# Kernel tuning notes

Hardware: AMD Instinct MI355X
Metric: run time of the kernel (lower is better)

Reference implementation:

```python
import jax, jax.numpy as jnp
import numpy as np

N = 4096          # nodes
E = 131072        # edges (avg degree 32)
D_IN = 128        # node_dim
H = 256           # hidden_dim
HEADS = 8
DH = H // HEADS


def setup_inputs() -> dict:
    key = jax.random.key(0)
    ks = jax.random.split(key, 24)
    w = lambda k, shape: (jax.random.normal(k, shape, dtype=jnp.float32) * 0.05)
    inp = {
        "x": jax.random.normal(ks[0], (N, D_IN), dtype=jnp.float32),
        "edge_index": jax.random.randint(ks[1], (2, E), 0, N, dtype=jnp.int32),
        # GCN conv weights (PyG GCNConv: out = aggr(norm * x @ W) + b)
        "W1": w(ks[2], (D_IN, H)), "b1": jnp.zeros((H,), jnp.float32),
        "W2": w(ks[3], (H, H)),    "b2": jnp.zeros((H,), jnp.float32),
        "W3": w(ks[4], (H, H)),    "b3": jnp.zeros((H,), jnp.float32),
        # nn.MultiheadAttention params (torch layout: y = x @ W.T + b)
        "in_w": w(ks[5], (3 * H, H)), "in_b": jnp.zeros((3 * H,), jnp.float32),
        "out_w": w(ks[6], (H, H)),    "out_b": jnp.zeros((H,), jnp.float32),
        # failure_predictor MLP: H -> H/2 -> 3
        "fp1_w": w(ks[7], (H // 2, H)), "fp1_b": jnp.zeros((H // 2,), jnp.float32),
        "fp2_w": w(ks[8], (3, H // 2)), "fp2_b": jnp.zeros((3,), jnp.float32),
        # pattern_detector MLP: H -> H/2 -> 10
        "pd1_w": w(ks[9], (H // 2, H)),  "pd1_b": jnp.zeros((H // 2,), jnp.float32),
        "pd2_w": w(ks[10], (10, H // 2)), "pd2_b": jnp.zeros((10,), jnp.float32),
    }
    return inp


def gcn_conv(x, src, dst, W, b):
    """PyG GCNConv with self-loops and symmetric normalization."""
    h = x @ W                                   # [N, H]
    deg = jnp.zeros((N,), x.dtype).at[dst].add(1.0) + 1.0   # +1 for self-loop
    dinv = jax.lax.rsqrt(deg)
    norm = dinv[src] * dinv[dst]                # [E]
    agg = jnp.zeros_like(h).at[dst].add(h[src] * norm[:, None])
    agg = agg + h * (1.0 / deg)[:, None]        # self-loop term: deg^-1/2 * deg^-1/2
    return agg + b


def mha(h, in_w, in_b, out_w, out_b):
    qkv = h @ in_w.T + in_b                     # [N, 3H]
    q, k, v = jnp.split(qkv, 3, axis=-1)
    q = q.reshape(N, HEADS, DH).transpose(1, 0, 2)   # [h, N, dh]
    k = k.reshape(N, HEADS, DH).transpose(1, 0, 2)
    v = v.reshape(N, HEADS, DH).transpose(1, 0, 2)
    scores = jnp.einsum("hnd,hmd->hnm", q, k) / np.sqrt(DH)
    attn = jax.nn.softmax(scores, axis=-1)
    o = jnp.einsum("hnm,hmd->hnd", attn, v)          # [h, N, dh]
    o = o.transpose(1, 0, 2).reshape(N, H)
    return o @ out_w.T + out_b


def reference(x, edge_index, W1, b1, W2, b2, W3, b3, in_w, in_b, out_w, out_b,
              fp1_w, fp1_b, fp2_w, fp2_b, pd1_w, pd1_b, pd2_w, pd2_b):
    src, dst = edge_index[0], edge_index[1]
    h = jax.nn.relu(gcn_conv(x, src, dst, W1, b1))   # dropout is identity in eval
    h = jax.nn.relu(gcn_conv(h, src, dst, W2, b2))
    h = gcn_conv(h, src, dst, W3, b3)
    h = h + mha(h, in_w, in_b, out_w, out_b)
    risk = jax.nn.softmax(jax.nn.relu(h @ fp1_w.T + fp1_b) @ fp2_w.T + fp2_b, axis=-1)
    patterns = jax.nn.sigmoid(jax.nn.relu(h @ pd1_w.T + pd1_b) @ pd2_w.T + pd2_b)
    return risk, patterns
```

## Files before the change

### kernel.cpp

```cpp
#include <hip/hip_runtime.h>
#include <math.h>

static constexpr int NNODE = 4096;
static constexpr int HDIM  = 256;
static constexpr int DIN   = 128;
static constexpr int HEADS = 8;
static constexpr int SPLIT = 2;

using short8 = __attribute__((ext_vector_type(8))) short;
using f32x4  = __attribute__((ext_vector_type(4))) float;

__device__ inline unsigned short bfr(float x) {
    union { float f; unsigned u; } v; v.f = x;
    unsigned r = v.u + 0x7FFFu + ((v.u >> 16) & 1u);
    return (unsigned short)(r >> 16);
}
__device__ inline unsigned cvt_pk_bf16(float lo, float hi) {
    unsigned r;
    asm("v_cvt_pk_bf16_f32 %0, %1, %2" : "=v"(r) : "v"(lo), "v"(hi));
    return r;
}

__global__ void k_deg(const int* __restrict__ ei, int* __restrict__ degi, int E) {
    int e = blockIdx.x * 256 + threadIdx.x;
    if (e < E) atomicAdd(&degi[ei[E + e]], 1);
}

__global__ __launch_bounds__(256) void k_scan_norm(const int* __restrict__ degi,
        int* __restrict__ off, int* __restrict__ cursor,
        float* __restrict__ dinv, float* __restrict__ invdeg) {
    __shared__ int partial[256];
    __shared__ int basesh[256];
    int t = threadIdx.x;
    int local[16];
    int s = 0;
    #pragma unroll
    for (int i = 0; i < 16; ++i) { local[i] = degi[t * 16 + i]; s += local[i]; }
    partial[t] = s;
    __syncthreads();
    if (t == 0) {
        int run = 0;
        for (int i = 0; i < 256; ++i) { basesh[i] = run; run += partial[i]; }
    }
    __syncthreads();
    int b = basesh[t];
    #pragma unroll
    for (int i = 0; i < 16; ++i) {
        int n = t * 16 + i;
        off[n] = b; cursor[n] = b; b += local[i];
        float d = (float)local[i] + 1.0f;
        dinv[n]   = rsqrtf(d);
        invdeg[n] = 1.0f / d;
    }
}

__global__ void k_fill(const int* __restrict__ ei, int* __restrict__ cursor,
                       int* __restrict__ csr, int E) {
    int e = blockIdx.x * 256 + threadIdx.x;
    if (e < E) {
        int d = ei[E + e];
        int p = atomicAdd(&cursor[d], 1);
        csr[p] = ei[e];
    }
}

__global__ __launch_bounds__(256) void k_prep(
        const float* __restrict__ W1, const float* __restrict__ W2,
        const float* __restrict__ W3, const float* __restrict__ in_w,
        const float* __restrict__ outw, const float* __restrict__ fp1w,
        const float* __restrict__ pd1w, const float* __restrict__ fp1b,
        const float* __restrict__ pd1b,
        unsigned short* __restrict__ W1t, unsigned short* __restrict__ W2t,
        unsigned short* __restrict__ W3t, unsigned short* __restrict__ in_wb,
        unsigned short* __restrict__ outwb, unsigned short* __restrict__ wcatb,
        float* __restrict__ bcat) {
    int idx = blockIdx.x * 256 + threadIdx.x;
    if (idx < 32768) {
        int c = idx >> 7, k = idx & 127;
        W1t[idx] = bfr(W1[(size_t)k * 256 + c]);
    } else if (idx < 98304) {
        int j = idx - 32768; int c = j >> 8, k = j & 255;
        W2t[j] = bfr(W2[(size_t)k * 256 + c]);
    } else if (idx < 163840) {
        int j = idx - 98304; int c = j >> 8, k = j & 255;
        W3t[j] = bfr(W3[(size_t)k * 256 + c]);
    } else if (idx < 360448) {
        int j = idx - 163840;
        in_wb[j] = bfr(in_w[j]);
    } else if (idx < 425984) {
        int j = idx - 360448;
        outwb[j] = bfr(outw[j]);
    } else {
        int j = idx - 425984;
        int row = j >> 8, k = j & 255;
        wcatb[j] = bfr(row < 128 ? fp1w[(size_t)row * 256 + k]
                                 : pd1w[(size_t)(row - 128) * 256 + k]);
        if (j < 256) bcat[j] = (j < 128) ? fp1b[j] : pd1b[j - 128];
    }
}

__global__ __launch_bounds__(256) void k_cvt_x(const float* __restrict__ x,
                                               unsigned short* __restrict__ xb) {
    int i = (blockIdx.x * 256 + threadIdx.x) * 8;
    float4 a = *(const float4*)&x[i];
    float4 b = *(const float4*)&x[i + 4];
    short8 o;
    o[0]=(short)bfr(a.x); o[1]=(short)bfr(a.y); o[2]=(short)bfr(a.z); o[3]=(short)bfr(a.w);
    o[4]=(short)bfr(b.x); o[5]=(short)bfr(b.y); o[6]=(short)bfr(b.z); o[7]=(short)bfr(b.w);
    *(short8*)&xb[i] = o;
}

template<int K, int EPI, bool BIAS, bool ADD>
__global__ __launch_bounds__(256) void k_bgemm(
        const unsigned short* __restrict__ A, const unsigned short* __restrict__ B,
        const float* __restrict__ bias, const float* __restrict__ addsrc,
        void* __restrict__ P0, void* __restrict__ P1, void* __restrict__ P2,
        int Nout) {
    const int lane = threadIdx.x & 63, wave = threadIdx.x >> 6;
    const int ql = lane & 15, g = lane >> 4;
    const int m0w = blockIdx.y * 64 + wave * 16;
    const int n0 = blockIdx.x * 64;
    const unsigned short* ap = A + (size_t)(m0w + ql) * K + g * 8;
    const unsigned short* bp = B + (size_t)(n0 + ql) * K + g * 8;

    f32x4 acc[4] = {{0,0,0,0},{0,0,0,0},{0,0,0,0},{0,0,0,0}};
    #pragma unroll 4
    for (int k0 = 0; k0 < K; k0 += 32) {
        short8 a = *(const short8*)(ap + k0);
        #pragma unroll
        for (int nt = 0; nt < 4; ++nt) {
            short8 b = *(const short8*)(bp + (size_t)nt * 16 * K + k0);
            acc[nt] = __builtin_amdgcn_mfma_f32_16x16x32_bf16(a, b, acc[nt], 0, 0, 0);
        }
    }
    #pragma unroll
    for (int nt = 0; nt < 4; ++nt) {
        const int col = n0 + nt * 16 + ql;
        const float bv = BIAS ? bias[col] : 0.f;
        if (EPI == 2) {
            const int sec = col >> 8, cc = col & 255;
            const int head = cc >> 5, dh = cc & 31;
            unsigned short* dst = (unsigned short*)(sec == 0 ? P0 : (sec == 1 ? P1 : P2));
            const float sc = (sec == 0) ? 0.17677669529663687f : 1.0f;
            #pragma unroll
            for (int i = 0; i < 4; ++i) {
                int row = m0w + g * 4 + i;
                dst[((size_t)head * NNODE + row) * 32 + dh] = bfr((acc[nt][i] + bv) * sc);
            }
        } else if (EPI == 1) {
            unsigned short* Cb = (unsigned short*)P0;
            #pragma unroll
            for (int i = 0; i < 4; ++i) {
                int row = m0w + g * 4 + i;
                float v = acc[nt][i] + bv;
                if (ADD) v += addsrc[(size_t)row * Nout + col];
                Cb[(size_t)row * Nout + col] = bfr(v);
            }
        } else {
            float* Cf = (float*)P0;
            #pragma unroll
            for (int i = 0; i < 4; ++i) {
                int row = m0w + g * 4 + i;
                float v = acc[nt][i] + bv;
                if (ADD) v += addsrc[(size_t)row * Nout + col];
                Cf[(size_t)row * Nout + col] = v;
            }
        }
    }
}

template<int MODE>
__global__ __launch_bounds__(256) void k_gather(const float* __restrict__ hW,
        const int* __restrict__ csr, const int* __restrict__ off,
        const int* __restrict__ degi, const float* __restrict__ dinv,
        const float* __restrict__ invdeg, const float* __restrict__ bias,
        float* __restrict__ aggf, unsigned short* __restrict__ aggb) {
    const int n = blockIdx.x;
    const int c = threadIdx.x;
    const int start = off[n];
    const int cnt = degi[n];
    __shared__ int   sidx[64];
    __shared__ float swht[64];
    float acc = 0.f;
    for (int k0 = 0; k0 < cnt; k0 += 64) {
        __syncthreads();
        if (c < 64 && k0 + c < cnt) {
            int s = csr[start + k0 + c];
            sidx[c] = s;
            swht[c] = dinv[s];
        }
        __syncthreads();
        int lim = min(64, cnt - k0);
        for (int k = 0; k < lim; ++k)
            acc += hW[(size_t)sidx[k] * HDIM + c] * swht[k];
    }
    float val = acc * dinv[n] + hW[(size_t)n * HDIM + c] * invdeg[n] + bias[c];
    if (MODE == 0) {
        aggb[(size_t)n * HDIM + c] = bfr(fmaxf(val, 0.f));
    } else {
        aggf[(size_t)n * HDIM + c] = val;
        aggb[(size_t)n * HDIM + c] = bfr(val);
    }
}

__global__ __launch_bounds__(256) void k_attn_mfma(const unsigned short* __restrict__ qh,
        const unsigned short* __restrict__ kh, const unsigned short* __restrict__ vh,
        float* __restrict__ po, float* __restrict__ pm, float* __restrict__ pl) {
    const int hd = blockIdx.x;
    const int qb = blockIdx.y;
    const int z  = blockIdx.z;
    const int tid = threadIdx.x;
    const int wave = tid >> 6, lane = tid & 63;
    const int ql = lane & 15, g = lane >> 4;

    __shared__ unsigned short Klds[64 * 40];
    __shared__ unsigned short Vt[32 * 72];
    __shared__ unsigned short Plds[4][16 * 72];

    const unsigned short* khh = kh + (size_t)hd * NNODE * 32;
    const unsigned short* vhh = vh + (size_t)hd * NNODE * 32;
    const int row = qb * 64 + wave * 16 + ql;

    short8 qf = *(const short8*)(qh + ((size_t)hd * NNODE + row) * 32 + g * 8);

    f32x4 oa0 = {0,0,0,0}, oa1 = {0,0,0,0};
    float m = -INFINITY, l = 0.f;

    const int skey = tid >> 2, sdh = (tid & 3) * 8;
    const int vkey = tid & 63, vdh = (tid >> 6) * 8;

    const int t0 = z * (NNODE / 64 / SPLIT);
    const int t1 = t0 + (NNODE / 64 / SPLIT);
    for (int kt = t0; kt < t1; ++kt) {
        __syncthreads();
        {
            short8 kv = *(const short8*)(khh + (size_t)(kt * 64 + skey) * 32 + sdh);
            *(short8*)&Klds[skey * 40 + sdh] = kv;
            short8 vv = *(const short8*)(vhh + (size_t)(kt * 64 + vkey) * 32 + vdh);
            #pragma unroll
            for (int i = 0; i < 8; ++i)
                Vt[(vdh + i) * 72 + vkey] = (unsigned short)vv[i];
        }
        __syncthreads();

        f32x4 st[4];
        #pragma unroll
        for (int t = 0; t < 4; ++t) {
            short8 kf = *(const short8*)&Klds[(t * 16 + ql) * 40 + g * 8];
            st[t] = __builtin_amdgcn_mfma_f32_16x16x32_bf16(kf, qf, (f32x4){0.f,0.f,0.f,0.f}, 0, 0, 0);
        }

        float mloc = -INFINITY;
        #pragma unroll
        for (int t = 0; t < 4; ++t)
            mloc = fmaxf(mloc, fmaxf(fmaxf(st[t][0], st[t][1]), fmaxf(st[t][2], st[t][3])));
        mloc = fmaxf(mloc, __shfl_xor(mloc, 16));
        mloc = fmaxf(mloc, __shfl_xor(mloc, 32));

        if (!__all(mloc <= m + 8.f)) {
            float mnew = fmaxf(m, mloc);
            float corr = __expf(m - mnew);
            l *= corr;
            oa0 *= corr;
            oa1 *= corr;
            m = mnew;
        }

        float ll = 0.f;
        unsigned pw[8];
        #pragma unroll
        for (int t = 0; t < 4; ++t) {
            float p0 = __expf(st[t][0] - m);
            float p1 = __expf(st[t][1] - m);
            float p2 = __expf(st[t][2] - m);
            float p3 = __expf(st[t][3] - m);
            ll += (p0 + p1) + (p2 + p3);
            pw[t * 2 + 0] = cvt_pk_bf16(p0, p1);
            pw[t * 2 + 1] = cvt_pk_bf16(p2, p3);
        }
        ll += __shfl_xor(ll, 16);
        ll += __shfl_xor(ll, 32);
        l += ll;

        #pragma unroll
        for (int t = 0; t < 4; ++t) {
            uint2 w2; w2.x = pw[t * 2 + 0]; w2.y = pw[t * 2 + 1];
            *(uint2*)&Plds[wave][ql * 72 + t * 16 + g * 4] = w2;
        }

        #pragma unroll
        for (int c = 0; c < 2; ++c) {
            short8 pf = *(const short8*)&Plds[wave][ql * 72 + c * 32 + g * 8];
            short8 v0 = *(const short8*)&Vt[ql * 72 + c * 32 + g * 8];
            short8 v1 = *(const short8*)&Vt[(16 + ql) * 72 + c * 32 + g * 8];
            oa0 = __builtin_amdgcn_mfma_f32_16x16x32_bf16(v0, pf, oa0, 0, 0, 0);
            oa1 = __builtin_amdgcn_mfma_f32_16x16x32_bf16(v1, pf, oa1, 0, 0, 0);
        }
    }

    const size_t pidx = ((size_t)hd * NNODE + row) * SPLIT + z;
    float* pp = po + pidx * 32;
    float4 r0 = {oa0[0], oa0[1], oa0[2], oa0[3]};
    float4 r1 = {oa1[0], oa1[1], oa1[2], oa1[3]};
    *(float4*)&pp[g * 4]      = r0;
    *(float4*)&pp[16 + g * 4] = r1;
    if (g == 0) { pm[pidx] = m; pl[pidx] = l; }
}

__global__ __launch_bounds__(256) void k_attn_merge(const float* __restrict__ po,
        const float* __restrict__ pm, const float* __restrict__ pl,
        unsigned short* __restrict__ ob) {
    int idx = blockIdx.x * 256 + threadIdx.x;
    int row = idx >> 8, c = idx & 255;
    int hd = c >> 5, dh = c & 31;
    size_t base = ((size_t)hd * NNODE + row) * SPLIT;
    float m0 = pm[base], m1 = pm[base + 1];
    float M = fmaxf(m0, m1);
    float w0 = __expf(m0 - M), w1 = __expf(m1 - M);
    float L = pl[base] * w0 + pl[base + 1] * w1;
    float v = (po[base * 32 + dh] * w0 + po[(base + 1) * 32 + dh] * w1) / L;
    ob[idx] = bfr(v);
}

__global__ __launch_bounds__(256) void k_heads2(const float* __restrict__ th,
        const float* __restrict__ fp2w, const float* __restrict__ fp2b,
        const float* __restrict__ pd2w, const float* __restrict__ pd2b,
        float* __restrict__ out) {
    const int wave = threadIdx.x >> 6, lane = threadIdx.x & 63;
    const int n = blockIdx.x * 4 + wave;
    const int half = lane >> 5;
    const int li = lane & 31;
    float4 h4 = *(const float4*)&th[(size_t)n * HDIM + half * 128 + li * 4];
    h4.x = fmaxf(h4.x, 0.f); h4.y = fmaxf(h4.y, 0.f);
    h4.z = fmaxf(h4.z, 0.f); h4.w = fmaxf(h4.w, 0.f);
    float lf[3];
    float lp[10];
    #pragma unroll
    for (int j = 0; j < 10; ++j) {
        float partial = 0.f;
        if (half == 0) {
            if (j < 3) {
                float4 wv = *(const float4*)&fp2w[j * 128 + li * 4];
                partial = h4.x*wv.x + h4.y*wv.y + h4.z*wv.z + h4.w*wv.w;
            }
        } else {
            float4 wv = *(const float4*)&pd2w[j * 128 + li * 4];
            partial = h4.x*wv.x + h4.y*wv.y + h4.z*wv.z + h4.w*wv.w;
        }
        #pragma unroll
        for (int d = 1; d < 32; d <<= 1) partial += __shfl_xor(partial, d);
        if (j < 3) lf[j] = partial;
        lp[j] = partial;
    }
    if (lane == 0) {
        float l0 = lf[0] + fp2b[0], l1 = lf[1] + fp2b[1], l2 = lf[2] + fp2b[2];
        float mx = fmaxf(l0, fmaxf(l1, l2));
        float e0 = __expf(l0 - mx), e1 = __expf(l1 - mx), e2 = __expf(l2 - mx);
        float inv = 1.f / (e0 + e1 + e2);
        out[(size_t)n * 3 + 0] = e0 * inv;
        out[(size_t)n * 3 + 1] = e1 * inv;
        out[(size_t)n * 3 + 2] = e2 * inv;
    } else if (lane == 32) {
        #pragma unroll
        for (int j = 0; j < 10; ++j)
            out[(size_t)NNODE * 3 + (size_t)n * 10 + j] =
                1.f / (1.f + __expf(-(lp[j] + pd2b[j])));
    }
}

extern "C" void kernel_launch(void* const* d_in, const int* in_sizes, int n_in,
                              void* d_out, int out_size, void* d_ws, size_t ws_size,
                              hipStream_t stream) {
    const float* x    = (const float*)d_in[0];
    const int*   ei   = (const int*)  d_in[1];
    const float* W1   = (const float*)d_in[2];
    const float* b1   = (const float*)d_in[3];
    const float* W2   = (const float*)d_in[4];
    const float* b2   = (const float*)d_in[5];
    const float* W3   = (const float*)d_in[6];
    const float* b3   = (const float*)d_in[7];
    const float* in_w = (const float*)d_in[8];
    const float* in_b = (const float*)d_in[9];
    const float* outw = (const float*)d_in[10];
    const float* outb = (const float*)d_in[11];
    const float* fp1w = (const float*)d_in[12];
    const float* fp1b = (const float*)d_in[13];
    const float* fp2w = (const float*)d_in[14];
    const float* fp2b = (const float*)d_in[15];
    const float* pd1w = (const float*)d_in[16];
    const float* pd1b = (const float*)d_in[17];
    const float* pd2w = (const float*)d_in[18];
    const float* pd2b = (const float*)d_in[19];
    float* out = (float*)d_out;

    const int E = in_sizes[1] / 2;

    char* w = (char*)d_ws;
    auto alloc = [&](size_t bytes) {
        char* p = w; w += (bytes + 255) & ~(size_t)255; return p;
    };
    int*   degi   = (int*)alloc(NNODE * 4);
    int*   off    = (int*)alloc(NNODE * 4);
    int*   cursor = (int*)alloc(NNODE * 4);
    int*   csr    = (int*)alloc((size_t)E * 4);
    float* dinv   = (float*)alloc(NNODE * 4);
    float* invdeg = (float*)alloc(NNODE * 4);
    unsigned short* W1t   = (unsigned short*)alloc(256 * 128 * 2);
    unsigned short* W2t   = (unsigned short*)alloc(256 * 256 * 2);
    unsigned short* W3t   = (unsigned short*)alloc(256 * 256 * 2);
    unsigned short* in_wb = (unsigned short*)alloc(768 * 256 * 2);
    unsigned short* outwb = (unsigned short*)alloc(256 * 256 * 2);
    unsigned short* wcatb = (unsigned short*)alloc(256 * 256 * 2);
    float* bcat  = (float*)alloc(256 * 4);
    unsigned short* xb    = (unsigned short*)alloc((size_t)NNODE * DIN * 2);
    float* bufA  = (float*)alloc((size_t)NNODE * HDIM * 4);
    unsigned short* aggb1 = (unsigned short*)alloc((size_t)NNODE * HDIM * 2);
    unsigned short* aggb2 = (unsigned short*)alloc((size_t)NNODE * HDIM * 2);
    float* hf    = (float*)alloc((size_t)NNODE * HDIM * 4);
    unsigned short* hb    = (unsigned short*)alloc((size_t)NNODE * HDIM * 2);
    unsigned short* qh    = (unsigned short*)alloc((size_t)HEADS * NNODE * 32 * 2);
    unsigned short* kh    = (unsigned short*)alloc((size_t)HEADS * NNODE * 32 * 2);
    unsigned short* vh    = (unsigned short*)alloc((size_t)HEADS * NNODE * 32 * 2);
    float* po    = (float*)alloc((size_t)HEADS * NNODE * SPLIT * 32 * 4);
    float* pm    = (float*)alloc((size_t)HEADS * NNODE * SPLIT * 4);
    float* pl    = (float*)alloc((size_t)HEADS * NNODE * SPLIT * 4);
    unsigned short* ob    = (unsigned short*)alloc((size_t)NNODE * HDIM * 2);
    unsigned short* hfinb = (unsigned short*)alloc((size_t)NNODE * HDIM * 2);

    hipMemsetAsync(degi, 0, NNODE * sizeof(int), stream);
    k_deg<<<(E + 255) / 256, 256, 0, stream>>>(ei, degi, E);
    k_scan_norm<<<1, 256, 0, stream>>>(degi, off, cursor, dinv, invdeg);
    k_fill<<<(E + 255) / 256, 256, 0, stream>>>(ei, cursor, csr, E);
    k_prep<<<1920, 256, 0, stream>>>(W1, W2, W3, in_w, outw, fp1w, pd1w, fp1b, pd1b,
                                     W1t, W2t, W3t, in_wb, outwb, wcatb, bcat);
    k_cvt_x<<<(NNODE * DIN / 8) / 256, 256, 0, stream>>>(x, xb);

    dim3 g256(4, 64);
    dim3 g768(12, 64);

    k_bgemm<DIN, 0, false, false><<<g256, 256, 0, stream>>>(xb, W1t, nullptr, nullptr, bufA, nullptr, nullptr, HDIM);
    k_gather<0><<<NNODE, 256, 0, stream>>>(bufA, csr, off, degi, dinv, invdeg, b1, nullptr, aggb1);
    k_bgemm<HDIM, 0, false, false><<<g256, 256, 0, stream>>>(aggb1, W2t, nullptr, nullptr, bufA, nullptr, nullptr, HDIM);
    k_gather<0><<<NNODE, 256, 0, stream>>>(bufA, csr, off, degi, dinv, invdeg, b2, nullptr, aggb2);
    k_bgemm<HDIM, 0, false, false><<<g256, 256, 0, stream>>>(aggb2, W3t, nullptr, nullptr, bufA, nullptr, nullptr, HDIM);
    k_gather<1><<<NNODE, 256, 0, stream>>>(bufA, csr, off, degi, dinv, invdeg, b3, hf, hb);

    k_bgemm<HDIM, 2, true, false><<<g768, 256, 0, stream>>>(hb, in_wb, in_b, nullptr, qh, kh, vh, 768);
    k_attn_mfma<<<dim3(HEADS, NNODE / 64, SPLIT), 256, 0, stream>>>(qh, kh, vh, po, pm, pl);
    k_attn_merge<<<(NNODE * HDIM) / 256, 256, 0, stream>>>(po, pm, pl, ob);
    k_bgemm<HDIM, 1, true, true><<<g256, 256, 0, stream>>>(ob, outwb, outb, hf, hfinb, nullptr, nullptr, HDIM);

    k_bgemm<HDIM, 0, true, false><<<g256, 256, 0, stream>>>(hfinb, wcatb, bcat, nullptr, bufA, nullptr, nullptr, HDIM);
    k_heads2<<<NNODE / 4, 256, 0, stream>>>(bufA, fp2w, fp2b, pd2w, pd2b, out);
}
```

Before: 208.1 us.

## Use bf16 intermediates, exp2 softmax, split-4 attention, narrower GEMM tiles, fused prep

The GCN features produced by each GEMM are now stored as bf16 and converted back in the gather, halving gather traffic. The attention kernel folds log2(e) into the Q scale so it can use exp2. It raises the key split to 4, reads K directly from global memory instead of LDS, double-buffers V in LDS and writes bf16 partial outputs. The GEMM tile width drops from 64 to 32 columns for more blocks, and the x conversion is folded into the weight prep kernel to remove a launch. The trade-offs are lower precision in the intermediates and partials, and more partial merge work.

```diff
diff --git a/kernel.cpp b/kernel.cpp
--- a/kernel.cpp
+++ b/kernel.cpp
@@ -5,7 +5,7 @@
 static constexpr int HDIM  = 256;
 static constexpr int DIN   = 128;
 static constexpr int HEADS = 8;
-static constexpr int SPLIT = 2;
+static constexpr int SPLIT = 4;
 
 using short8 = __attribute__((ext_vector_type(8))) short;
 using f32x4  = __attribute__((ext_vector_type(4))) float;
@@ -15,11 +15,16 @@
     unsigned r = v.u + 0x7FFFu + ((v.u >> 16) & 1u);
     return (unsigned short)(r >> 16);
 }
+__device__ inline float bf2f(unsigned short u) {
+    union { unsigned u; float f; } v; v.u = (unsigned)u << 16; return v.f;
+}
 __device__ inline unsigned cvt_pk_bf16(float lo, float hi) {
     unsigned r;
     asm("v_cvt_pk_bf16_f32 %0, %1, %2" : "=v"(r) : "v"(lo), "v"(hi));
     return r;
 }
+
+static constexpr float QSCALE_LOG2 = 0.25503527f;
 
 __global__ void k_deg(const int* __restrict__ ei, int* __restrict__ degi, int E) {
     int e = blockIdx.x * 256 + threadIdx.x;
@@ -69,11 +74,11 @@
         const float* __restrict__ W3, const float* __restrict__ in_w,
         const float* __restrict__ outw, const float* __restrict__ fp1w,
         const float* __restrict__ pd1w, const float* __restrict__ fp1b,
-        const float* __restrict__ pd1b,
+        const float* __restrict__ pd1b, const float* __restrict__ x,
         unsigned short* __restrict__ W1t, unsigned short* __restrict__ W2t,
         unsigned short* __restrict__ W3t, unsigned short* __restrict__ in_wb,
         unsigned short* __restrict__ outwb, unsigned short* __restrict__ wcatb,
-        float* __restrict__ bcat) {
+        float* __restrict__ bcat, unsigned short* __restrict__ xb) {
     int idx = blockIdx.x * 256 + threadIdx.x;
     if (idx < 32768) {
         int c = idx >> 7, k = idx & 127;
@@ -90,24 +95,21 @@
     } else if (idx < 425984) {
         int j = idx - 360448;
         outwb[j] = bfr(outw[j]);
-    } else {
+    } else if (idx < 491520) {
         int j = idx - 425984;
         int row = j >> 8, k = j & 255;
         wcatb[j] = bfr(row < 128 ? fp1w[(size_t)row * 256 + k]
                                  : pd1w[(size_t)(row - 128) * 256 + k]);
         if (j < 256) bcat[j] = (j < 128) ? fp1b[j] : pd1b[j - 128];
-    }
-}
-
-__global__ __launch_bounds__(256) void k_cvt_x(const float* __restrict__ x,
-                                               unsigned short* __restrict__ xb) {
-    int i = (blockIdx.x * 256 + threadIdx.x) * 8;
-    float4 a = *(const float4*)&x[i];
-    float4 b = *(const float4*)&x[i + 4];
-    short8 o;
-    o[0]=(short)bfr(a.x); o[1]=(short)bfr(a.y); o[2]=(short)bfr(a.z); o[3]=(short)bfr(a.w);
-    o[4]=(short)bfr(b.x); o[5]=(short)bfr(b.y); o[6]=(short)bfr(b.z); o[7]=(short)bfr(b.w);
-    *(short8*)&xb[i] = o;
+    } else if (idx < 557056) {
+        int i = (idx - 491520) * 8;
+        float4 a = *(const float4*)&x[i];
+        float4 b = *(const float4*)&x[i + 4];
+        short8 o;
+        o[0]=(short)bfr(a.x); o[1]=(short)bfr(a.y); o[2]=(short)bfr(a.z); o[3]=(short)bfr(a.w);
+        o[4]=(short)bfr(b.x); o[5]=(short)bfr(b.y); o[6]=(short)bfr(b.z); o[7]=(short)bfr(b.w);
+        *(short8*)&xb[i] = o;
+    }
 }
 
 template<int K, int EPI, bool BIAS, bool ADD>
@@ -119,29 +121,29 @@
     const int lane = threadIdx.x & 63, wave = threadIdx.x >> 6;
     const int ql = lane & 15, g = lane >> 4;
     const int m0w = blockIdx.y * 64 + wave * 16;
-    const int n0 = blockIdx.x * 64;
+    const int n0 = blockIdx.x * 32;
     const unsigned short* ap = A + (size_t)(m0w + ql) * K + g * 8;
     const unsigned short* bp = B + (size_t)(n0 + ql) * K + g * 8;
 
-    f32x4 acc[4] = {{0,0,0,0},{0,0,0,0},{0,0,0,0},{0,0,0,0}};
-    #pragma unroll 4
+    f32x4 acc[2] = {{0,0,0,0},{0,0,0,0}};
+    #pragma unroll
     for (int k0 = 0; k0 < K; k0 += 32) {
         short8 a = *(const short8*)(ap + k0);
         #pragma unroll
-        for (int nt = 0; nt < 4; ++nt) {
+        for (int nt = 0; nt < 2; ++nt) {
             short8 b = *(const short8*)(bp + (size_t)nt * 16 * K + k0);
             acc[nt] = __builtin_amdgcn_mfma_f32_16x16x32_bf16(a, b, acc[nt], 0, 0, 0);
         }
     }
     #pragma unroll
-    for (int nt = 0; nt < 4; ++nt) {
+    for (int nt = 0; nt < 2; ++nt) {
         const int col = n0 + nt * 16 + ql;
         const float bv = BIAS ? bias[col] : 0.f;
         if (EPI == 2) {
             const int sec = col >> 8, cc = col & 255;
             const int head = cc >> 5, dh = cc & 31;
             unsigned short* dst = (unsigned short*)(sec == 0 ? P0 : (sec == 1 ? P1 : P2));
-            const float sc = (sec == 0) ? 0.17677669529663687f : 1.0f;
+            const float sc = (sec == 0) ? QSCALE_LOG2 : 1.0f;
             #pragma unroll
             for (int i = 0; i < 4; ++i) {
                 int row = m0w + g * 4 + i;
@@ -170,7 +172,7 @@
 }
 
 template<int MODE>
-__global__ __launch_bounds__(256) void k_gather(const float* __restrict__ hW,
+__global__ __launch_bounds__(256) void k_gather(const unsigned short* __restrict__ hW,
         const int* __restrict__ csr, const int* __restrict__ off,
         const int* __restrict__ degi, const float* __restrict__ dinv,
         const float* __restrict__ invdeg, const float* __restrict__ bias,
@@ -192,9 +194,9 @@
         __syncthreads();
         int lim = min(64, cnt - k0);
         for (int k = 0; k < lim; ++k)
-            acc += hW[(size_t)sidx[k] * HDIM + c] * swht[k];
-    }
-    float val = acc * dinv[n] + hW[(size_t)n * HDIM + c] * invdeg[n] + bias[c];
+            acc += bf2f(hW[(size_t)sidx[k] * HDIM + c]) * swht[k];
+    }
+    float val = acc * dinv[n] + bf2f(hW[(size_t)n * HDIM + c]) * invdeg[n] + bias[c];
     if (MODE == 0) {
         aggb[(size_t)n * HDIM + c] = bfr(fmaxf(val, 0.f));
     } else {
@@ -205,7 +207,7 @@
 
 __global__ __launch_bounds__(256) void k_attn_mfma(const unsigned short* __restrict__ qh,
         const unsigned short* __restrict__ kh, const unsigned short* __restrict__ vh,
-        float* __restrict__ po, float* __restrict__ pm, float* __restrict__ pl) {
+        unsigned short* __restrict__ po, float* __restrict__ pm, float* __restrict__ pl) {
     const int hd = blockIdx.x;
     const int qb = blockIdx.y;
     const int z  = blockIdx.z;
@@ -213,41 +215,41 @@
     const int wave = tid >> 6, lane = tid & 63;
     const int ql = lane & 15, g = lane >> 4;
 
-    __shared__ unsigned short Klds[64 * 40];
-    __shared__ unsigned short Vt[32 * 72];
+    __shared__ unsigned short Vt[2][32 * 72];
     __shared__ unsigned short Plds[4][16 * 72];
 
     const unsigned short* khh = kh + (size_t)hd * NNODE * 32;
     const unsigned short* vhh = vh + (size_t)hd * NNODE * 32;
     const int row = qb * 64 + wave * 16 + ql;
-
     short8 qf = *(const short8*)(qh + ((size_t)hd * NNODE + row) * 32 + g * 8);
 
     f32x4 oa0 = {0,0,0,0}, oa1 = {0,0,0,0};
     float m = -INFINITY, l = 0.f;
 
-    const int skey = tid >> 2, sdh = (tid & 3) * 8;
     const int vkey = tid & 63, vdh = (tid >> 6) * 8;
-
-    const int t0 = z * (NNODE / 64 / SPLIT);
-    const int t1 = t0 + (NNODE / 64 / SPLIT);
-    for (int kt = t0; kt < t1; ++kt) {
-        __syncthreads();
-        {
-            short8 kv = *(const short8*)(khh + (size_t)(kt * 64 + skey) * 32 + sdh);
-            *(short8*)&Klds[skey * 40 + sdh] = kv;
-            short8 vv = *(const short8*)(vhh + (size_t)(kt * 64 + vkey) * 32 + vdh);
+    const int TPS = NNODE / 64 / SPLIT;
+    const int t0 = z * TPS;
+
+    {
+        short8 vv = *(const short8*)(vhh + (size_t)(t0 * 64 + vkey) * 32 + vdh);
+        #pragma unroll
+        for (int i = 0; i < 8; ++i) Vt[0][(vdh + i) * 72 + vkey] = (unsigned short)vv[i];
+    }
+    __syncthreads();
+    int cur = 0;
+
+    for (int kt = t0; kt < t0 + TPS; ++kt) {
+        if (kt + 1 < t0 + TPS) {
+            short8 vv = *(const short8*)(vhh + (size_t)((kt + 1) * 64 + vkey) * 32 + vdh);
             #pragma unroll
-            for (int i = 0; i < 8; ++i)
-                Vt[(vdh + i) * 72 + vkey] = (unsigned short)vv[i];
-        }
-        __syncthreads();
+            for (int i = 0; i < 8; ++i) Vt[cur ^ 1][(vdh + i) * 72 + vkey] = (unsigned short)vv[i];
+        }
 
         f32x4 st[4];
         #pragma unroll
         for (int t = 0; t < 4; ++t) {
-            short8 kf = *(const short8*)&Klds[(t * 16 + ql) * 40 + g * 8];
-            st[t] = __builtin_amdgcn_mfma_f32_16x16x32_bf16(kf, qf, (f32x4){0.f,0.f,0.f,0.f}, 0, 0, 0);
+            short8 kf = *(const short8*)(khh + (size_t)(kt * 64 + t * 16 + ql) * 32 + g * 8);
+            st[t] = __builtin_amdgcn_mfma_f32_16x16x32_bf16(kf, qf, (f32x4){0,0,0,0}, 0, 0, 0);
         }
 
         float mloc = -INFINITY;
@@ -259,21 +261,18 @@
 
         if (!__all(mloc <= m + 8.f)) {
             float mnew = fmaxf(m, mloc);
-            float corr = __expf(m - mnew);
-            l *= corr;
-            oa0 *= corr;
-            oa1 *= corr;
-            m = mnew;
+            float corr = exp2f(m - mnew);
+            l *= corr; oa0 *= corr; oa1 *= corr; m = mnew;
         }
 
         float ll = 0.f;
         unsigned pw[8];
         #pragma unroll
         for (int t = 0; t < 4; ++t) {
-            float p0 = __expf(st[t][0] - m);
-            float p1 = __expf(st[t][1] - m);
-            float p2 = __expf(st[t][2] - m);
-            float p3 = __expf(st[t][3] - m);
+            float p0 = exp2f(st[t][0] - m);
+            float p1 = exp2f(st[t][1] - m);
+            float p2 = exp2f(st[t][2] - m);
+            float p3 = exp2f(st[t][3] - m);
             ll += (p0 + p1) + (p2 + p3);
             pw[t * 2 + 0] = cvt_pk_bf16(p0, p1);
             pw[t * 2 + 1] = cvt_pk_bf16(p2, p3);
@@ -291,35 +290,40 @@
         #pragma unroll
         for (int c = 0; c < 2; ++c) {
             short8 pf = *(const short8*)&Plds[wave][ql * 72 + c * 32 + g * 8];
-            short8 v0 = *(const short8*)&Vt[ql * 72 + c * 32 + g * 8];
-            short8 v1 = *(const short8*)&Vt[(16 + ql) * 72 + c * 32 + g * 8];
+            short8 v0 = *(const short8*)&Vt[cur][ql * 72 + c * 32 + g * 8];
+            short8 v1 = *(const short8*)&Vt[cur][(16 + ql) * 72 + c * 32 + g * 8];
             oa0 = __builtin_amdgcn_mfma_f32_16x16x32_bf16(v0, pf, oa0, 0, 0, 0);
             oa1 = __builtin_amdgcn_mfma_f32_16x16x32_bf16(v1, pf, oa1, 0, 0, 0);
         }
+        __syncthreads();
+        cur ^= 1;
     }
 
     const size_t pidx = ((size_t)hd * NNODE + row) * SPLIT + z;
-    float* pp = po + pidx * 32;
-    float4 r0 = {oa0[0], oa0[1], oa0[2], oa0[3]};
-    float4 r1 = {oa1[0], oa1[1], oa1[2], oa1[3]};
-    *(float4*)&pp[g * 4]      = r0;
-    *(float4*)&pp[16 + g * 4] = r1;
+    unsigned short* pp = po + pidx * 32;
+    uint2 r0, r1;
+    r0.x = cvt_pk_bf16(oa0[0], oa0[1]); r0.y = cvt_pk_bf16(oa0[2], oa0[3]);
+    r1.x = cvt_pk_bf16(oa1[0], oa1[1]); r1.y = cvt_pk_bf16(oa1[2], oa1[3]);
+    *(uint2*)&pp[g * 4]      = r0;
+    *(uint2*)&pp[16 + g * 4] = r1;
     if (g == 0) { pm[pidx] = m; pl[pidx] = l; }
 }
 
-__global__ __launch_bounds__(256) void k_attn_merge(const float* __restrict__ po,
+__global__ __launch_bounds__(256) void k_attn_merge(const unsigned short* __restrict__ po,
         const float* __restrict__ pm, const float* __restrict__ pl,
         unsigned short* __restrict__ ob) {
     int idx = blockIdx.x * 256 + threadIdx.x;
     int row = idx >> 8, c = idx & 255;
     int hd = c >> 5, dh = c & 31;
-    size_t base = ((size_t)hd * NNODE + row) * SPLIT;
-    float m0 = pm[base], m1 = pm[base + 1];
-    float M = fmaxf(m0, m1);
-    float w0 = __expf(m0 - M), w1 = __expf(m1 - M);
-    float L = pl[base] * w0 + pl[base + 1] * w1;
-    float v = (po[base * 32 + dh] * w0 + po[(base + 1) * 32 + dh] * w1) / L;
-    ob[idx] = bfr(v);
+    size_t b4 = ((size_t)hd * NNODE + row) * SPLIT;
+    float m0 = pm[b4+0], m1 = pm[b4+1], m2 = pm[b4+2], m3 = pm[b4+3];
+    float M = fmaxf(fmaxf(m0, m1), fmaxf(m2, m3));
+    float w0 = exp2f(m0 - M), w1 = exp2f(m1 - M);
+    float w2 = exp2f(m2 - M), w3 = exp2f(m3 - M);
+    float L = pl[b4]*w0 + pl[b4+1]*w1 + pl[b4+2]*w2 + pl[b4+3]*w3;
+    float v = bf2f(po[(b4+0)*32 + dh])*w0 + bf2f(po[(b4+1)*32 + dh])*w1
+            + bf2f(po[(b4+2)*32 + dh])*w2 + bf2f(po[(b4+3)*32 + dh])*w3;
+    ob[idx] = bfr(v / L);
 }
 
 __global__ __launch_bounds__(256) void k_heads2(const float* __restrict__ th,
@@ -414,6 +418,7 @@
     float* bcat  = (float*)alloc(256 * 4);
     unsigned short* xb    = (unsigned short*)alloc((size_t)NNODE * DIN * 2);
     float* bufA  = (float*)alloc((size_t)NNODE * HDIM * 4);
+    unsigned short* bufAb = (unsigned short*)alloc((size_t)NNODE * HDIM * 2);
     unsigned short* aggb1 = (unsigned short*)alloc((size_t)NNODE * HDIM * 2);
     unsigned short* aggb2 = (unsigned short*)alloc((size_t)NNODE * HDIM * 2);
     float* hf    = (float*)alloc((size_t)NNODE * HDIM * 4);
@@ -421,7 +426,7 @@
     unsigned short* qh    = (unsigned short*)alloc((size_t)HEADS * NNODE * 32 * 2);
     unsigned short* kh    = (unsigned short*)alloc((size_t)HEADS * NNODE * 32 * 2);
     unsigned short* vh    = (unsigned short*)alloc((size_t)HEADS * NNODE * 32 * 2);
-    float* po    = (float*)alloc((size_t)HEADS * NNODE * SPLIT * 32 * 4);
+    unsigned short* po    = (unsigned short*)alloc((size_t)HEADS * NNODE * SPLIT * 32 * 2);
     float* pm    = (float*)alloc((size_t)HEADS * NNODE * SPLIT * 4);
     float* pl    = (float*)alloc((size_t)HEADS * NNODE * SPLIT * 4);
     unsigned short* ob    = (unsigned short*)alloc((size_t)NNODE * HDIM * 2);
@@ -431,19 +436,18 @@
     k_deg<<<(E + 255) / 256, 256, 0, stream>>>(ei, degi, E);
     k_scan_norm<<<1, 256, 0, stream>>>(degi, off, cursor, dinv, invdeg);
     k_fill<<<(E + 255) / 256, 256, 0, stream>>>(ei, cursor, csr, E);
-    k_prep<<<1920, 256, 0, stream>>>(W1, W2, W3, in_w, outw, fp1w, pd1w, fp1b, pd1b,
-                                     W1t, W2t, W3t, in_wb, outwb, wcatb, bcat);
-    k_cvt_x<<<(NNODE * DIN / 8) / 256, 256, 0, stream>>>(x, xb);
-
-    dim3 g256(4, 64);
-    dim3 g768(12, 64);
-
-    k_bgemm<DIN, 0, false, false><<<g256, 256, 0, stream>>>(xb, W1t, nullptr, nullptr, bufA, nullptr, nullptr, HDIM);
-    k_gather<0><<<NNODE, 256, 0, stream>>>(bufA, csr, off, degi, dinv, invdeg, b1, nullptr, aggb1);
-    k_bgemm<HDIM, 0, false, false><<<g256, 256, 0, stream>>>(aggb1, W2t, nullptr, nullptr, bufA, nullptr, nullptr, HDIM);
-    k_gather<0><<<NNODE, 256, 0, stream>>>(bufA, csr, off, degi, dinv, invdeg, b2, nullptr, aggb2);
-    k_bgemm<HDIM, 0, false, false><<<g256, 256, 0, stream>>>(aggb2, W3t, nullptr, nullptr, bufA, nullptr, nullptr, HDIM);
-    k_gather<1><<<NNODE, 256, 0, stream>>>(bufA, csr, off, degi, dinv, invdeg, b3, hf, hb);
+    k_prep<<<2176, 256, 0, stream>>>(W1, W2, W3, in_w, outw, fp1w, pd1w, fp1b, pd1b, x,
+                                     W1t, W2t, W3t, in_wb, outwb, wcatb, bcat, xb);
+
+    dim3 g256(HDIM / 32, NNODE / 64);
+    dim3 g768(768 / 32, NNODE / 64);
+
+    k_bgemm<DIN, 1, false, false><<<g256, 256, 0, stream>>>(xb, W1t, nullptr, nullptr, bufAb, nullptr, nullptr, HDIM);
+    k_gather<0><<<NNODE, 256, 0, stream>>>(bufAb, csr, off, degi, dinv, invdeg, b1, nullptr, aggb1);
+    k_bgemm<HDIM, 1, false, false><<<g256, 256, 0, stream>>>(aggb1, W2t, nullptr, nullptr, bufAb, nullptr, nullptr, HDIM);
+    k_gather<0><<<NNODE, 256, 0, stream>>>(bufAb, csr, off, degi, dinv, invdeg, b2, nullptr, aggb2);
+    k_bgemm<HDIM, 1, false, false><<<g256, 256, 0, stream>>>(aggb2, W3t, nullptr, nullptr, bufAb, nullptr, nullptr, HDIM);
+    k_gather<1><<<NNODE, 256, 0, stream>>>(bufAb, csr, off, degi, dinv, invdeg, b3, hf, hb);
 
     k_bgemm<HDIM, 2, true, false><<<g768, 256, 0, stream>>>(hb, in_wb, in_b, nullptr, qh, kh, vh, 768);
     k_attn_mfma<<<dim3(HEADS, NNODE / 64, SPLIT), 256, 0, stream>>>(qh, kh, vh, po, pm, pl);
```

Measured after the change: 206.4 us. About the same (-0.8%).
